# Performance work log

Hardware: AMD Instinct MI355X
Metric: run time of the kernel (lower is better)

The kernel has to match this reference:

```python
import jax, jax.numpy as jnp
import numpy as np

N_NODES = 50000


def gcn_conv(x, W, b, src, dst, n_nodes):
    # PyG GCNConv: y = D^-1/2 (A + I) D^-1/2 (x @ W) + b, with D counting self-loops
    h = x @ W                                             # [N, out]
    deg = jnp.ones((n_nodes,), h.dtype).at[dst].add(1.0)  # in-degree + self-loop
    dinv = jax.lax.rsqrt(deg)
    norm = dinv[src] * dinv[dst]                          # [E]
    msg = h[src] * norm[:, None]                          # [E, out]
    out = jnp.zeros_like(h).at[dst].add(msg)              # scatter-add over edges
    out = out + h * (dinv * dinv)[:, None]                # self-loop contribution
    return out + b


def setup_inputs() -> dict:
    key = jax.random.key(0)
    k = jax.random.split(key, 7)
    d_in, d_hid, d_out = 128, 128, 64
    x = jax.random.normal(k[0], (N_NODES, d_in), jnp.float32)
    edge_index = jax.random.randint(k[1], (2, 800000), 0, N_NODES, jnp.int64)
    s1 = 1.0 / np.sqrt(d_in)
    s2 = 1.0 / np.sqrt(d_hid)
    W1 = jax.random.uniform(k[2], (d_in, d_hid), jnp.float32, -s1, s1)
    b1 = jnp.zeros((d_hid,), jnp.float32)
    W2 = jax.random.uniform(k[3], (d_hid, d_out), jnp.float32, -s2, s2)
    b2 = jnp.zeros((d_out,), jnp.float32)
    return {"x": x, "edge_index": edge_index, "W1": W1, "b1": b1, "W2": W2, "b2": b2}


def reference(x, edge_index, W1, b1, W2, b2):
    src, dst = edge_index[0], edge_index[1]
    h = jax.nn.relu(gcn_conv(x, W1, b1, src, dst, N_NODES))
    h = gcn_conv(h, W2, b2, src, dst, N_NODES)
    return jax.nn.log_softmax(h, axis=1)
```

## Files before the change

### kernel.cpp

```cpp
#include <hip/hip_runtime.h>
#include <hip/hip_bf16.h>
#include <math.h>


typedef unsigned int uint32;
typedef unsigned short ushort16;
typedef __attribute__((ext_vector_type(8))) short bf16x8;
typedef __attribute__((ext_vector_type(4))) float f32x4;

__device__ inline unsigned short f2bf_rne(float f) {
    uint32 x = __float_as_uint(f);
    uint32 r = (x + 0x7fffu + ((x >> 16) & 1u)) >> 16;
    return (unsigned short)r;
}
__device__ inline uint32 pack_bf16x2(float a, float b) {
    return (uint32)f2bf_rne(a) | ((uint32)f2bf_rne(b) << 16);
}
__device__ inline float2 unpack_bf16x2(uint32 u) {
    float2 r;
    r.x = __uint_as_float(u << 16);
    r.y = __uint_as_float(u & 0xffff0000u);
    return r;
}

#define NHB 128

__global__ __launch_bounds__(256) void hist_conv_k(const int* __restrict__ dst, int E,
                                                   int NW, int chunk,
                                                   uint32* __restrict__ counts_pb,
                                                   ushort16* __restrict__ rankx,
                                                   const float* __restrict__ W1,
                                                   const float* __restrict__ W2,
                                                   unsigned short* __restrict__ W1t,
                                                   unsigned short* __restrict__ W2t) {
    const int tid = threadIdx.x;
    if ((int)blockIdx.x >= NHB) {
        int idx = ((int)blockIdx.x - NHB) * 256 + tid;
        if (idx < 128 * 128) {
            int ns = idx >> 7, k = idx & 127;
            int t = ns >> 4, m = ns & 15;
            int col = 32 * (t >> 1) + 2 * m + (t & 1);
            W1t[idx] = f2bf_rne(W1[k * 128 + col]);
        } else {
            int i2 = idx - 128 * 128;
            if (i2 < 64 * 128) {
                int ns = i2 >> 7, k = i2 & 127;
                int t = ns >> 4, m = ns & 15;
                int col = 32 * (t >> 1) + 2 * m + (t & 1);
                W2t[i2] = f2bf_rne(W2[k * 64 + col]);
            }
        }
        return;
    }
    extern __shared__ uint32 sh[];
    const int b = blockIdx.x;
    for (int i = tid; i < NW; i += 256) sh[i] = 0;
    __syncthreads();
    const int e0 = b * chunk;
    const int e1 = min(E, e0 + chunk);
    int e = e0 + tid;
    for (; e + 768 < e1; e += 1024) {
        int d0 = dst[e];
        int d1 = dst[e + 256];
        int d2 = dst[e + 512];
        int d3 = dst[e + 768];
        uint32 o0 = atomicAdd(&sh[d0 >> 1], (d0 & 1) ? 0x10000u : 1u);
        uint32 o1 = atomicAdd(&sh[d1 >> 1], (d1 & 1) ? 0x10000u : 1u);
        uint32 o2 = atomicAdd(&sh[d2 >> 1], (d2 & 1) ? 0x10000u : 1u);
        uint32 o3 = atomicAdd(&sh[d3 >> 1], (d3 & 1) ? 0x10000u : 1u);
        rankx[e]       = (ushort16)((d0 & 1) ? (o0 >> 16) : (o0 & 0xffffu));
        rankx[e + 256] = (ushort16)((d1 & 1) ? (o1 >> 16) : (o1 & 0xffffu));
        rankx[e + 512] = (ushort16)((d2 & 1) ? (o2 >> 16) : (o2 & 0xffffu));
        rankx[e + 768] = (ushort16)((d3 & 1) ? (o3 >> 16) : (o3 & 0xffffu));
    }
    for (; e < e1; e += 256) {
        int d = dst[e];
        uint32 o = atomicAdd(&sh[d >> 1], (d & 1) ? 0x10000u : 1u);
        rankx[e] = (ushort16)((d & 1) ? (o >> 16) : (o & 0xffffu));
    }
    __syncthreads();
    uint32* dstp = counts_pb + (size_t)b * NW;
    for (int i = tid; i < NW; i += 256) dstp[i] = sh[i];
}

__global__ __launch_bounds__(256) void scan2_k(const uint32* __restrict__ counts_pb,
                                               int N, int NW,
                                               ushort16* __restrict__ basecum,
                                               int* __restrict__ exscan,
                                               int* __restrict__ blocksum,
                                               float* __restrict__ dinv) {
    __shared__ int sd[256];
    const int tid = threadIdx.x;
    const int n   = blockIdx.x * 256 + tid;
    const int nc  = n < N ? n : N - 1;
    const int w   = nc >> 1;
    const bool hi = (nc & 1) != 0;
    int cum = 0;
    for (int bb = 0; bb < NHB; bb += 16) {
        uint32 wv[16];
#pragma unroll
        for (int j = 0; j < 16; ++j)
            wv[j] = counts_pb[(size_t)(bb + j) * NW + w];
#pragma unroll
        for (int j = 0; j < 16; ++j) {
            int c = hi ? (int)(wv[j] >> 16) : (int)(wv[j] & 0xffffu);
            if (n < N) basecum[(size_t)(bb + j) * N + n] = (ushort16)cum;
            cum += c;
        }
    }
    int v = (n < N) ? cum : 0;
    if (n < N) dinv[n] = rsqrtf((float)(v + 1));
    sd[tid] = v;
    __syncthreads();
    for (int off = 1; off < 256; off <<= 1) {
        int t = (tid >= off) ? sd[tid - off] : 0;
        __syncthreads();
        sd[tid] += t;
        __syncthreads();
    }
    if (n < N) exscan[n] = sd[tid] - v;
    if (tid == 255) blocksum[blockIdx.x] = sd[255];
}

__global__ __launch_bounds__(256) void blocksums_finalize_k(const int* __restrict__ blocksum,
                                                            int NB,
                                                            const int* __restrict__ exscan,
                                                            int N,
                                                            int* __restrict__ offsets) {
    __shared__ int sd[256];
    __shared__ int boff;
    const int tid = threadIdx.x;
    int v = (tid < NB) ? blocksum[tid] : 0;
    sd[tid] = v;
    __syncthreads();
    for (int off = 1; off < 256; off <<= 1) {
        int t = (tid >= off) ? sd[tid - off] : 0;
        __syncthreads();
        sd[tid] += t;
        __syncthreads();
    }
    if (tid == 0) boff = sd[blockIdx.x] - blocksum[blockIdx.x];
    __syncthreads();
    const int gid = blockIdx.x * 256 + tid;
    if (gid < N) offsets[gid] = boff + exscan[gid];
    if (blockIdx.x == 0 && tid == 0) offsets[N] = sd[255];
}

__global__ __launch_bounds__(256) void fill_gemm1_k(const int* __restrict__ src,
                                                    const int* __restrict__ dst, int E,
                                                    int chunk, int N,
                                                    const ushort16* __restrict__ rankx,
                                                    const ushort16* __restrict__ basecum,
                                                    const int* __restrict__ offsets,
                                                    ushort16* __restrict__ csr_src,
                                                    const float* __restrict__ X,
                                                    const unsigned short* __restrict__ Wt,
                                                    const float* __restrict__ dinv,
                                                    uint32* __restrict__ Yu, int Nrows) {
    if ((int)blockIdx.x < 256) {
        const int f  = blockIdx.x;
        const int b  = f >> 1;
        const ushort16* bc = basecum + (size_t)b * N;
        const int q2 = chunk >> 1;
        const int e0 = b * chunk + (f & 1) * q2;
        const int e1 = min(E, e0 + q2);
        int e = e0 + threadIdx.x;
        for (; e + 768 < e1; e += 1024) {
#pragma unroll
            for (int j = 0; j < 4; ++j) {
                int ej = e + j * 256;
                int d = dst[ej];
                int pos = offsets[d] + (int)bc[d] + (int)rankx[ej];
                csr_src[pos] = (ushort16)src[ej];
            }
        }
        for (; e < e1; e += 256) {
            int d = dst[e];
            int pos = offsets[d] + (int)bc[d] + (int)rankx[e];
            csr_src[pos] = (ushort16)src[e];
        }
        return;
    }
    constexpr int NCOL = 128;
    constexpr int NT = NCOL / 16;
    const int tid  = threadIdx.x;
    const int wave = tid >> 6;
    const int lane = tid & 63;
    const int m16  = lane & 15;
    const int q    = lane >> 4;
    const int r0   = ((int)blockIdx.x - 256) * 64 + wave * 16;

    int arow = r0 + m16;
    if (arow >= Nrows) arow = Nrows - 1;

    bf16x8 afrag[4];
#pragma unroll
    for (int kb = 0; kb < 4; ++kb) {
        const float* p = &X[(size_t)arow * 128 + kb * 32 + q * 8];
        float4 u0 = *(const float4*)p;
        float4 u1 = *(const float4*)(p + 4);
        bf16x8 a;
        a[0] = (short)f2bf_rne(u0.x); a[1] = (short)f2bf_rne(u0.y);
        a[2] = (short)f2bf_rne(u0.z); a[3] = (short)f2bf_rne(u0.w);
        a[4] = (short)f2bf_rne(u1.x); a[5] = (short)f2bf_rne(u1.y);
        a[6] = (short)f2bf_rne(u1.z); a[7] = (short)f2bf_rne(u1.w);
        afrag[kb] = a;
    }

    f32x4 acc[NT];
#pragma unroll
    for (int t = 0; t < NT; ++t) acc[t] = (f32x4){0.f, 0.f, 0.f, 0.f};
#pragma unroll
    for (int t = 0; t < NT; ++t) {
        const unsigned short* Bp = &Wt[(size_t)(t * 16 + m16) * 128 + q * 8];
#pragma unroll
        for (int kb = 0; kb < 4; ++kb) {
            bf16x8 bfrag = *(const bf16x8*)&Bp[kb * 32];
            acc[t] = __builtin_amdgcn_mfma_f32_16x16x32_bf16(afrag[kb], bfrag, acc[t], 0, 0, 0);
        }
    }
#pragma unroll
    for (int i = 0; i < 4; ++i) {
        int row = r0 + q * 4 + i;
        if (row < Nrows) {
            float dn = dinv[row];
#pragma unroll
            for (int u = 0; u < NT / 2; ++u)
                Yu[(size_t)row * (NCOL / 2) + u * 16 + m16] =
                    pack_bf16x2(acc[2 * u][i] * dn, acc[2 * u + 1][i] * dn);
        }
    }
}

__global__ __launch_bounds__(256) void mfma_gemm2_k(const unsigned short* __restrict__ X,
                                                    const unsigned short* __restrict__ Wt,
                                                    const float* __restrict__ dinv,
                                                    uint32* __restrict__ Yu, int Nrows) {
    constexpr int NCOL = 64;
    constexpr int NT = NCOL / 16;
    const int tid  = threadIdx.x;
    const int wave = tid >> 6;
    const int lane = tid & 63;
    const int m16  = lane & 15;
    const int q    = lane >> 4;
    const int r0   = blockIdx.x * 64 + wave * 16;

    int arow = r0 + m16;
    if (arow >= Nrows) arow = Nrows - 1;

    bf16x8 afrag[4];
#pragma unroll
    for (int kb = 0; kb < 4; ++kb)
        afrag[kb] = *(const bf16x8*)&X[(size_t)arow * 128 + kb * 32 + q * 8];

    f32x4 acc[NT];
#pragma unroll
    for (int t = 0; t < NT; ++t) acc[t] = (f32x4){0.f, 0.f, 0.f, 0.f};
#pragma unroll
    for (int t = 0; t < NT; ++t) {
        const unsigned short* Bp = &Wt[(size_t)(t * 16 + m16) * 128 + q * 8];
#pragma unroll
        for (int kb = 0; kb < 4; ++kb) {
            bf16x8 bfrag = *(const bf16x8*)&Bp[kb * 32];
            acc[t] = __builtin_amdgcn_mfma_f32_16x16x32_bf16(afrag[kb], bfrag, acc[t], 0, 0, 0);
        }
    }
#pragma unroll
    for (int i = 0; i < 4; ++i) {
        int row = r0 + q * 4 + i;
        if (row < Nrows) {
            float dn = dinv[row];
#pragma unroll
            for (int u = 0; u < NT / 2; ++u)
                Yu[(size_t)row * (NCOL / 2) + u * 16 + m16] =
                    pack_bf16x2(acc[2 * u][i] * dn, acc[2 * u + 1][i] * dn);
        }
    }
}

__global__ __launch_bounds__(256) void agg1_k(const unsigned short* __restrict__ hs,
                                              const int* __restrict__ offsets,
                                              const ushort16* __restrict__ csr_src,
                                              const float* __restrict__ dinv,
                                              const float* __restrict__ b1,
                                              unsigned short* __restrict__ out, int N) {
    const int tid  = threadIdx.x;
    const int node = blockIdx.x * 4 + (tid >> 6);
    const int lane = tid & 63;
    if (node >= N) return;
    const uint32* T = (const uint32*)hs;
    const int start = offsets[node];
    const int end   = offsets[node + 1];
    const float dn  = dinv[node];
    float2 self = unpack_bf16x2(T[(size_t)node * 64 + lane]);
    float ax0 = self.x, ay0 = self.y;
    float ax1 = 0.f, ay1 = 0.f, ax2 = 0.f, ay2 = 0.f, ax3 = 0.f, ay3 = 0.f;
    int p = start;
    for (; p + 3 < end; p += 4) {
        int s0 = csr_src[p];
        int s1 = csr_src[p + 1];
        int s2 = csr_src[p + 2];
        int s3 = csr_src[p + 3];
        float2 f0 = unpack_bf16x2(T[(size_t)s0 * 64 + lane]);
        float2 f1 = unpack_bf16x2(T[(size_t)s1 * 64 + lane]);
        float2 f2 = unpack_bf16x2(T[(size_t)s2 * 64 + lane]);
        float2 f3 = unpack_bf16x2(T[(size_t)s3 * 64 + lane]);
        ax0 += f0.x; ay0 += f0.y;
        ax1 += f1.x; ay1 += f1.y;
        ax2 += f2.x; ay2 += f2.y;
        ax3 += f3.x; ay3 += f3.y;
    }
    for (; p < end; ++p) {
        float2 f = unpack_bf16x2(T[(size_t)csr_src[p] * 64 + lane]);
        ax1 += f.x; ay1 += f.y;
    }
    float2 bb = ((const float2*)b1)[lane];
    float vx = ((ax0 + ax1) + (ax2 + ax3)) * dn + bb.x;
    float vy = ((ay0 + ay1) + (ay2 + ay3)) * dn + bb.y;
    vx = vx > 0.f ? vx : 0.f;
    vy = vy > 0.f ? vy : 0.f;
    ((uint32*)out)[(size_t)node * 64 + lane] = pack_bf16x2(vx, vy);
}

__global__ __launch_bounds__(256) void agg2_k(const unsigned short* __restrict__ hs,
                                              const int* __restrict__ offsets,
                                              const ushort16* __restrict__ csr_src,
                                              const float* __restrict__ dinv,
                                              const float* __restrict__ b2,
                                              float* __restrict__ out, int N) {
    const int tid  = threadIdx.x;
    const int node = blockIdx.x * 8 + (tid >> 5);
    const int l    = tid & 31;
    if (node >= N) return;
    const uint32* T = (const uint32*)hs;
    const int start = offsets[node];
    const int end   = offsets[node + 1];
    const float dn  = dinv[node];
    float2 self = unpack_bf16x2(T[(size_t)node * 32 + l]);
    float ax0 = self.x, ay0 = self.y;
    float ax1 = 0.f, ay1 = 0.f, ax2 = 0.f, ay2 = 0.f, ax3 = 0.f, ay3 = 0.f;
    int p = start;
    for (; p + 3 < end; p += 4) {
        int s0 = csr_src[p];
        int s1 = csr_src[p + 1];
        int s2 = csr_src[p + 2];
        int s3 = csr_src[p + 3];
        float2 f0 = unpack_bf16x2(T[(size_t)s0 * 32 + l]);
        float2 f1 = unpack_bf16x2(T[(size_t)s1 * 32 + l]);
        float2 f2 = unpack_bf16x2(T[(size_t)s2 * 32 + l]);
        float2 f3 = unpack_bf16x2(T[(size_t)s3 * 32 + l]);
        ax0 += f0.x; ay0 += f0.y;
        ax1 += f1.x; ay1 += f1.y;
        ax2 += f2.x; ay2 += f2.y;
        ax3 += f3.x; ay3 += f3.y;
    }
    for (; p < end; ++p) {
        float2 f = unpack_bf16x2(T[(size_t)csr_src[p] * 32 + l]);
        ax1 += f.x; ay1 += f.y;
    }
    float2 bb = ((const float2*)b2)[l];
    float vx = ((ax0 + ax1) + (ax2 + ax3)) * dn + bb.x;
    float vy = ((ay0 + ay1) + (ay2 + ay3)) * dn + bb.y;
    float m = fmaxf(vx, vy);
#pragma unroll
    for (int off = 16; off > 0; off >>= 1) m = fmaxf(m, __shfl_xor(m, off, 64));
    float ex = __expf(vx - m) + __expf(vy - m);
    float ssum = ex;
#pragma unroll
    for (int off = 16; off > 0; off >>= 1) ssum += __shfl_xor(ssum, off, 64);
    float lse = m + __logf(ssum);
    float2 o = {vx - lse, vy - lse};
    ((float2*)out)[(size_t)node * 32 + l] = o;
}

extern "C" void kernel_launch(void* const* d_in, const int* in_sizes, int n_in,
                              void* d_out, int out_size, void* d_ws, size_t ws_size,
                              hipStream_t stream) {
    const float* x  = (const float*)d_in[0];
    const int*   ei = (const int*)d_in[1];
    const float* W1 = (const float*)d_in[2];
    const float* b1 = (const float*)d_in[3];
    const float* W2 = (const float*)d_in[4];
    const float* b2 = (const float*)d_in[5];
    float* out = (float*)d_out;

    const int N = in_sizes[0] / 128;
    const int E = in_sizes[1] / 2;
    const int* src = ei;
    const int* dst = ei + E;
    const int NB = (N + 255) / 256;
    const int NW = (N + 1) / 2;
    const int chunk = (E + NHB - 1) / NHB;

    char* ws = (char*)d_ws;
    auto alloc = [&](size_t bytes) -> char* {
        char* p = ws;
        ws += (bytes + 255) & ~(size_t)255;
        return p;
    };
    unsigned short* h1  = (unsigned short*)alloc((size_t)N * 128 * 2);
    unsigned short* h1a = (unsigned short*)alloc((size_t)N * 128 * 2);
    unsigned short* h2  = (unsigned short*)alloc((size_t)N * 64 * 2);
    uint32* counts_pb = (uint32*)alloc((size_t)NHB * NW * 4);
    ushort16* basecum = (ushort16*)alloc((size_t)NHB * N * 2);
    ushort16* rankx   = (ushort16*)alloc((size_t)E * 2);
    ushort16* csr_src = (ushort16*)alloc((size_t)E * 2);
    float* dinv     = (float*)alloc((size_t)N * 4);
    int*   exscan   = (int*)alloc((size_t)N * 4);
    int*   blocksum = (int*)alloc((size_t)NB * 4);
    int*   offsets  = (int*)alloc((size_t)(N + 1) * 4);
    unsigned short* W1t = (unsigned short*)alloc(128 * 128 * 2);
    unsigned short* W2t = (unsigned short*)alloc(64 * 128 * 2);

    const int GB = (N + 63) / 64;
    const int CB = (128 * 128 + 64 * 128 + 255) / 256;

    hist_conv_k<<<NHB + CB, 256, NW * 4, stream>>>(dst, E, NW, chunk, counts_pb, rankx,
                                                   W1, W2, W1t, W2t);
    scan2_k<<<NB, 256, 0, stream>>>(counts_pb, N, NW, basecum, exscan, blocksum, dinv);
    blocksums_finalize_k<<<NB, 256, 0, stream>>>(blocksum, NB, exscan, N, offsets);
    fill_gemm1_k<<<256 + GB, 256, 0, stream>>>(src, dst, E, chunk, N, rankx, basecum,
                                               offsets, csr_src, x, W1t, dinv,
                                               (uint32*)h1, N);
    agg1_k<<<(N + 3) / 4, 256, 0, stream>>>(h1, offsets, csr_src, dinv, b1, h1a, N);
    mfma_gemm2_k<<<GB, 256, 0, stream>>>(h1a, W2t, dinv, (uint32*)h2, N);
    agg2_k<<<(N + 7) / 8, 256, 0, stream>>>(h2, offsets, csr_src, dinv, b2, out, N);
}
```

Measured before the change: 209.8 us.

## Fuse block-sum finalize into CSR fill and layer-1 aggregation into GEMM2

```diff
diff --git a/kernel.cpp b/kernel.cpp
--- a/kernel.cpp
+++ b/kernel.cpp
@@ -122,61 +122,59 @@
     if (tid == 255) blocksum[blockIdx.x] = sd[255];
 }
 
-__global__ __launch_bounds__(256) void blocksums_finalize_k(const int* __restrict__ blocksum,
-                                                            int NB,
-                                                            const int* __restrict__ exscan,
-                                                            int N,
-                                                            int* __restrict__ offsets) {
-    __shared__ int sd[256];
-    __shared__ int boff;
-    const int tid = threadIdx.x;
-    int v = (tid < NB) ? blocksum[tid] : 0;
-    sd[tid] = v;
-    __syncthreads();
-    for (int off = 1; off < 256; off <<= 1) {
-        int t = (tid >= off) ? sd[tid - off] : 0;
-        __syncthreads();
-        sd[tid] += t;
-        __syncthreads();
-    }
-    if (tid == 0) boff = sd[blockIdx.x] - blocksum[blockIdx.x];
-    __syncthreads();
-    const int gid = blockIdx.x * 256 + tid;
-    if (gid < N) offsets[gid] = boff + exscan[gid];
-    if (blockIdx.x == 0 && tid == 0) offsets[N] = sd[255];
-}
-
 __global__ __launch_bounds__(256) void fill_gemm1_k(const int* __restrict__ src,
                                                     const int* __restrict__ dst, int E,
                                                     int chunk, int N,
                                                     const ushort16* __restrict__ rankx,
                                                     const ushort16* __restrict__ basecum,
-                                                    const int* __restrict__ offsets,
+                                                    const int* __restrict__ blocksum,
+                                                    int NB,
+                                                    const int* __restrict__ exscan,
+                                                    int* __restrict__ offsets,
                                                     ushort16* __restrict__ csr_src,
                                                     const float* __restrict__ X,
                                                     const unsigned short* __restrict__ Wt,
                                                     const float* __restrict__ dinv,
                                                     uint32* __restrict__ Yu, int Nrows) {
+    __shared__ int sd[256];
+    __shared__ int ebs[256];
+    __shared__ int total;
     if ((int)blockIdx.x < 256) {
-        const int f  = blockIdx.x;
+        const int f   = blockIdx.x;
+        const int tid = threadIdx.x;
+        int v = (tid < NB) ? blocksum[tid] : 0;
+        sd[tid] = v;
+        __syncthreads();
+        for (int off = 1; off < 256; off <<= 1) {
+            int t = (tid >= off) ? sd[tid - off] : 0;
+            __syncthreads();
+            sd[tid] += t;
+            __syncthreads();
+        }
+        ebs[tid] = sd[tid] - v;
+        if (tid == 255) total = sd[255];
+        __syncthreads();
+        int g = f * 256 + tid;
+        if (g < N) offsets[g] = ebs[g >> 8] + exscan[g];
+        else if (g == N) offsets[N] = total;
         const int b  = f >> 1;
         const ushort16* bc = basecum + (size_t)b * N;
         const int q2 = chunk >> 1;
         const int e0 = b * chunk + (f & 1) * q2;
         const int e1 = min(E, e0 + q2);
-        int e = e0 + threadIdx.x;
+        int e = e0 + tid;
         for (; e + 768 < e1; e += 1024) {
 #pragma unroll
             for (int j = 0; j < 4; ++j) {
                 int ej = e + j * 256;
                 int d = dst[ej];
-                int pos = offsets[d] + (int)bc[d] + (int)rankx[ej];
+                int pos = ebs[d >> 8] + exscan[d] + (int)bc[d] + (int)rankx[ej];
                 csr_src[pos] = (ushort16)src[ej];
             }
         }
         for (; e < e1; e += 256) {
             int d = dst[e];
-            int pos = offsets[d] + (int)bc[d] + (int)rankx[e];
+            int pos = ebs[d >> 8] + exscan[d] + (int)bc[d] + (int)rankx[e];
             csr_src[pos] = (ushort16)src[e];
         }
         return;
@@ -232,94 +230,84 @@
     }
 }
 
-__global__ __launch_bounds__(256) void mfma_gemm2_k(const unsigned short* __restrict__ X,
-                                                    const unsigned short* __restrict__ Wt,
-                                                    const float* __restrict__ dinv,
-                                                    uint32* __restrict__ Yu, int Nrows) {
-    constexpr int NCOL = 64;
-    constexpr int NT = NCOL / 16;
+__global__ __launch_bounds__(1024) void agg1_gemm2_k(const unsigned short* __restrict__ hs,
+                                                     const int* __restrict__ offsets,
+                                                     const ushort16* __restrict__ csr_src,
+                                                     const float* __restrict__ dinv,
+                                                     const float* __restrict__ b1,
+                                                     const unsigned short* __restrict__ W2t,
+                                                     uint32* __restrict__ Yu, int N) {
+    __shared__ uint32 srow[16 * 68];
     const int tid  = threadIdx.x;
-    const int wave = tid >> 6;
+    const int w    = tid >> 6;
     const int lane = tid & 63;
-    const int m16  = lane & 15;
-    const int q    = lane >> 4;
-    const int r0   = blockIdx.x * 64 + wave * 16;
-
-    int arow = r0 + m16;
-    if (arow >= Nrows) arow = Nrows - 1;
-
-    bf16x8 afrag[4];
-#pragma unroll
-    for (int kb = 0; kb < 4; ++kb)
-        afrag[kb] = *(const bf16x8*)&X[(size_t)arow * 128 + kb * 32 + q * 8];
-
-    f32x4 acc[NT];
-#pragma unroll
-    for (int t = 0; t < NT; ++t) acc[t] = (f32x4){0.f, 0.f, 0.f, 0.f};
-#pragma unroll
-    for (int t = 0; t < NT; ++t) {
-        const unsigned short* Bp = &Wt[(size_t)(t * 16 + m16) * 128 + q * 8];
+    const int base = (int)blockIdx.x * 16;
+    const int node = base + w;
+    if (node < N) {
+        const uint32* T = (const uint32*)hs;
+        const int start = offsets[node];
+        const int end   = offsets[node + 1];
+        const float dn  = dinv[node];
+        float2 self = unpack_bf16x2(T[(size_t)node * 64 + lane]);
+        float ax0 = self.x, ay0 = self.y;
+        float ax1 = 0.f, ay1 = 0.f, ax2 = 0.f, ay2 = 0.f, ax3 = 0.f, ay3 = 0.f;
+        int p = start;
+        for (; p + 3 < end; p += 4) {
+            int s0 = csr_src[p];
+            int s1 = csr_src[p + 1];
+            int s2 = csr_src[p + 2];
+            int s3 = csr_src[p + 3];
+            float2 f0 = unpack_bf16x2(T[(size_t)s0 * 64 + lane]);
+            float2 f1 = unpack_bf16x2(T[(size_t)s1 * 64 + lane]);
+            float2 f2 = unpack_bf16x2(T[(size_t)s2 * 64 + lane]);
+            float2 f3 = unpack_bf16x2(T[(size_t)s3 * 64 + lane]);
+            ax0 += f0.x; ay0 += f0.y;
+            ax1 += f1.x; ay1 += f1.y;
+            ax2 += f2.x; ay2 += f2.y;
+            ax3 += f3.x; ay3 += f3.y;
+        }
+        for (; p < end; ++p) {
+            float2 f = unpack_bf16x2(T[(size_t)csr_src[p] * 64 + lane]);
+            ax1 += f.x; ay1 += f.y;
+        }
+        float2 bb = ((const float2*)b1)[lane];
+        float vx = ((ax0 + ax1) + (ax2 + ax3)) * dn + bb.x;
+        float vy = ((ay0 + ay1) + (ay2 + ay3)) * dn + bb.y;
+        vx = vx > 0.f ? vx : 0.f;
+        vy = vy > 0.f ? vy : 0.f;
+        srow[w * 68 + lane] = pack_bf16x2(vx, vy);
+    } else {
+        srow[w * 68 + lane] = 0;
+    }
+    __syncthreads();
+    if (w < 2) {
+        const int m16 = lane & 15;
+        const int q   = lane >> 4;
+        bf16x8 afrag[4];
+#pragma unroll
+        for (int kb = 0; kb < 4; ++kb)
+            afrag[kb] = *(const bf16x8*)&srow[m16 * 68 + kb * 16 + q * 4];
+        f32x4 acc0 = (f32x4){0.f, 0.f, 0.f, 0.f};
+        f32x4 acc1 = (f32x4){0.f, 0.f, 0.f, 0.f};
+        const unsigned short* Bp0 = &W2t[(size_t)((2 * w) * 16 + m16) * 128 + q * 8];
+        const unsigned short* Bp1 = &W2t[(size_t)((2 * w + 1) * 16 + m16) * 128 + q * 8];
 #pragma unroll
         for (int kb = 0; kb < 4; ++kb) {
-            bf16x8 bfrag = *(const bf16x8*)&Bp[kb * 32];
-            acc[t] = __builtin_amdgcn_mfma_f32_16x16x32_bf16(afrag[kb], bfrag, acc[t], 0, 0, 0);
-        }
-    }
-#pragma unroll
-    for (int i = 0; i < 4; ++i) {
-        int row = r0 + q * 4 + i;
-        if (row < Nrows) {
-            float dn = dinv[row];
-#pragma unroll
-            for (int u = 0; u < NT / 2; ++u)
-                Yu[(size_t)row * (NCOL / 2) + u * 16 + m16] =
-                    pack_bf16x2(acc[2 * u][i] * dn, acc[2 * u + 1][i] * dn);
-        }
-    }
-}
-
-__global__ __launch_bounds__(256) void agg1_k(const unsigned short* __restrict__ hs,
-                                              const int* __restrict__ offsets,
-                                              const ushort16* __restrict__ csr_src,
-                                              const float* __restrict__ dinv,
-                                              const float* __restrict__ b1,
-                                              unsigned short* __restrict__ out, int N) {
-    const int tid  = threadIdx.x;
-    const int node = blockIdx.x * 4 + (tid >> 6);
-    const int lane = tid & 63;
-    if (node >= N) return;
-    const uint32* T = (const uint32*)hs;
-    const int start = offsets[node];
-    const int end   = offsets[node + 1];
-    const float dn  = dinv[node];
-    float2 self = unpack_bf16x2(T[(size_t)node * 64 + lane]);
-    float ax0 = self.x, ay0 = self.y;
-    float ax1 = 0.f, ay1 = 0.f, ax2 = 0.f, ay2 = 0.f, ax3 = 0.f, ay3 = 0.f;
-    int p = start;
-    for (; p + 3 < end; p += 4) {
-        int s0 = csr_src[p];
-        int s1 = csr_src[p + 1];
-        int s2 = csr_src[p + 2];
-        int s3 = csr_src[p + 3];
-        float2 f0 = unpack_bf16x2(T[(size_t)s0 * 64 + lane]);
-        float2 f1 = unpack_bf16x2(T[(size_t)s1 * 64 + lane]);
-        float2 f2 = unpack_bf16x2(T[(size_t)s2 * 64 + lane]);
-        float2 f3 = unpack_bf16x2(T[(size_t)s3 * 64 + lane]);
-        ax0 += f0.x; ay0 += f0.y;
-        ax1 += f1.x; ay1 += f1.y;
-        ax2 += f2.x; ay2 += f2.y;
-        ax3 += f3.x; ay3 += f3.y;
-    }
-    for (; p < end; ++p) {
-        float2 f = unpack_bf16x2(T[(size_t)csr_src[p] * 64 + lane]);
-        ax1 += f.x; ay1 += f.y;
-    }
-    float2 bb = ((const float2*)b1)[lane];
-    float vx = ((ax0 + ax1) + (ax2 + ax3)) * dn + bb.x;
-    float vy = ((ay0 + ay1) + (ay2 + ay3)) * dn + bb.y;
-    vx = vx > 0.f ? vx : 0.f;
-    vy = vy > 0.f ? vy : 0.f;
-    ((uint32*)out)[(size_t)node * 64 + lane] = pack_bf16x2(vx, vy);
+            bf16x8 b0 = *(const bf16x8*)&Bp0[kb * 32];
+            bf16x8 b1f = *(const bf16x8*)&Bp1[kb * 32];
+            acc0 = __builtin_amdgcn_mfma_f32_16x16x32_bf16(afrag[kb], b0, acc0, 0, 0, 0);
+            acc1 = __builtin_amdgcn_mfma_f32_16x16x32_bf16(afrag[kb], b1f, acc1, 0, 0, 0);
+        }
+#pragma unroll
+        for (int i = 0; i < 4; ++i) {
+            int row = base + q * 4 + i;
+            if (row < N) {
+                float dn2 = dinv[row];
+                Yu[(size_t)row * 32 + w * 16 + m16] =
+                    pack_bf16x2(acc0[i] * dn2, acc1[i] * dn2);
+            }
+        }
+    }
 }
 
 __global__ __launch_bounds__(256) void agg2_k(const unsigned short* __restrict__ hs,
@@ -399,7 +387,6 @@
         return p;
     };
     unsigned short* h1  = (unsigned short*)alloc((size_t)N * 128 * 2);
-    unsigned short* h1a = (unsigned short*)alloc((size_t)N * 128 * 2);
     unsigned short* h2  = (unsigned short*)alloc((size_t)N * 64 * 2);
     uint32* counts_pb = (uint32*)alloc((size_t)NHB * NW * 4);
     ushort16* basecum = (ushort16*)alloc((size_t)NHB * N * 2);
@@ -418,11 +405,10 @@
     hist_conv_k<<<NHB + CB, 256, NW * 4, stream>>>(dst, E, NW, chunk, counts_pb, rankx,
                                                    W1, W2, W1t, W2t);
     scan2_k<<<NB, 256, 0, stream>>>(counts_pb, N, NW, basecum, exscan, blocksum, dinv);
-    blocksums_finalize_k<<<NB, 256, 0, stream>>>(blocksum, NB, exscan, N, offsets);
     fill_gemm1_k<<<256 + GB, 256, 0, stream>>>(src, dst, E, chunk, N, rankx, basecum,
-                                               offsets, csr_src, x, W1t, dinv,
-                                               (uint32*)h1, N);
-    agg1_k<<<(N + 3) / 4, 256, 0, stream>>>(h1, offsets, csr_src, dinv, b1, h1a, N);
-    mfma_gemm2_k<<<GB, 256, 0, stream>>>(h1a, W2t, dinv, (uint32*)h2, N);
+                                               blocksum, NB, exscan, offsets, csr_src,
+                                               x, W1t, dinv, (uint32*)h1, N);
+    agg1_gemm2_k<<<(N + 15) / 16, 1024, 0, stream>>>(h1, offsets, csr_src, dinv, b1,
+                                                     W2t, (uint32*)h2, N);
     agg2_k<<<(N + 7) / 8, 256, 0, stream>>>(h2, offsets, csr_src, dinv, b2, out, N);
 }
```

After: 207.6 us. No clear change (-1.1%).
